# Kernel tuning notes

Hardware: AMD Instinct MI355X
Metric: run time of the kernel (lower is better)

## Reference

```python
import jax, jax.numpy as jnp
import numpy as np

B, H, S, D = 4, 16, 2048, 64


def setup_inputs() -> dict:
    key = jax.random.key(0)
    kq, kk, kv = jax.random.split(key, 3)
    Q = jax.random.normal(kq, (B, H, S, D), dtype=jnp.float32)
    K = jax.random.normal(kk, (B, H, S, D), dtype=jnp.float32)
    V = jax.random.normal(kv, (B, H, S, D), dtype=jnp.float32)
    mask = jnp.ones((1, 1, S, S), dtype=jnp.int32)
    return {"Q": Q, "K": K, "V": V, "mask": mask}


def reference(Q, K, V, mask):
    d_k = Q.shape[-1]
    scale = 1.0 / jnp.sqrt(jnp.asarray(d_k, dtype=Q.dtype))
    # [B, H, S, S] attention scores
    attn = jnp.einsum('bhqd,bhkd->bhqk', Q, K) * scale
    # mask == 0 -> -1e9 (matches torch boolean-index assignment)
    attn = jnp.where(mask == 0, jnp.asarray(-1e9, dtype=attn.dtype), attn)
    softmax_attn = jax.nn.softmax(attn, axis=-1)
    out = jnp.einsum('bhqk,bhkd->bhqd', softmax_attn, V)
    return out
```

## Files before the change

### kernel.cpp

```cpp
#include <hip/hip_runtime.h>

typedef __bf16 bf16;
typedef __attribute__((ext_vector_type(8))) __bf16 bf16x8;
typedef __attribute__((ext_vector_type(8))) ushort ushort8v;
typedef __attribute__((ext_vector_type(4))) ushort ushort4v;
typedef __attribute__((ext_vector_type(2))) uint uint2v;
typedef __attribute__((ext_vector_type(4))) float f32x4;

constexpr int S_LEN = 2048;
constexpr int DH    = 64;
constexpr int QBLK  = 128;
constexpr int KVBLK = 64;
constexpr int NWAVE = 4;
constexpr int NT    = S_LEN / KVBLK;
constexpr float QSCALE = 0.125f * 1.44269504088896f;
constexpr float NEG    = -1.44269504e9f;
constexpr float THR    = 8.0f;
constexpr size_t TILE_BYTES = (size_t)KVBLK * DH * 2;
constexpr size_t KV_BYTES   = (size_t)64 * NT * TILE_BYTES;

__device__ __forceinline__ ushort bfb(float f) {
  bf16 b = (bf16)f;
  return __builtin_bit_cast(ushort, b);
}
__device__ __forceinline__ int SWZ(int row) {
  return ((row & 7) ^ ((row >> 3) & 7)) << 4;
}
__device__ __forceinline__ uint cvtpk(float lo, float hi) {
  uint r;
  asm("v_cvt_pk_bf16_f32 %0, %1, %2" : "=v"(r) : "v"(lo), "v"(hi));
  return r;
}
__device__ __forceinline__ void gload16(const char* g, void* l) {
  __builtin_amdgcn_global_load_lds(
      (__attribute__((address_space(1))) void*)(g),
      (__attribute__((address_space(3))) void*)(l), 16, 0, 0);
}

__global__ __launch_bounds__(256)
void mask_flags(const int* __restrict__ M, uint* __restrict__ F) {
  const int qt = blockIdx.x;
  const int tid = threadIdx.x;
  const int r  = tid >> 2;
  const int c0 = (tid & 3) * 16;
  __shared__ int s[4];
  uint bits = 0;
  for (int kt = 0; kt < NT; ++kt) {
    const int* row = M + (size_t)(qt * 64 + r) * S_LEN + kt * 64 + c0;
    int ok = 1;
#pragma unroll
    for (int i = 0; i < 4; ++i) {
      int4 v = *(const int4*)(row + i * 4);
      ok &= (v.x != 0) & (v.y != 0) & (v.z != 0) & (v.w != 0);
    }
    ok = __all(ok) ? 1 : 0;
    if ((tid & 63) == 0) s[tid >> 6] = ok;
    __syncthreads();
    if (s[0] & s[1] & s[2] & s[3]) bits |= 1u << kt;
    __syncthreads();
  }
  if (tid == 0) F[qt] = bits;
}

__global__ __launch_bounds__(256)
void cvt_kv(const float* __restrict__ K, const float* __restrict__ V,
            char* __restrict__ kws, char* __restrict__ vws) {
  const int t = blockIdx.x, bh = blockIdx.y, tid = threadIdx.x;
  const float* Kb = K + ((size_t)bh * S_LEN + t * KVBLK) * DH;
  const float* Vb = V + ((size_t)bh * S_LEN + t * KVBLK) * DH;
  char* kd = kws + ((size_t)bh * NT + t) * TILE_BYTES;
  char* vd = vws + ((size_t)bh * NT + t) * TILE_BYTES;

  const int kr0 = tid >> 3, kc8 = tid & 7;
#pragma unroll
  for (int h = 0; h < 2; ++h) {
    const int row = kr0 + 32 * h;
    const float* kp = Kb + (size_t)row * DH + kc8 * 8;
    float4 a = *(const float4*)kp;
    float4 b = *(const float4*)(kp + 4);
    ushort8v pk;
    pk[0]=bfb(a.x); pk[1]=bfb(a.y); pk[2]=bfb(a.z); pk[3]=bfb(a.w);
    pk[4]=bfb(b.x); pk[5]=bfb(b.y); pk[6]=bfb(b.z); pk[7]=bfb(b.w);
    *(ushort8v*)(kd + row * 128 + ((kc8 * 16) ^ SWZ(row))) = pk;
  }
  const int vr = (tid >> 4) * 4, vc = (tid & 15) * 4;
  float rr[4][4];
#pragma unroll
  for (int i = 0; i < 4; ++i)
    *(float4*)rr[i] = *(const float4*)(Vb + (size_t)(vr + i) * DH + vc);
#pragma unroll
  for (int c = 0; c < 4; ++c) {
    const int d = vc + c;
    ushort4v p4;
    p4[0]=bfb(rr[0][c]); p4[1]=bfb(rr[1][c]);
    p4[2]=bfb(rr[2][c]); p4[3]=bfb(rr[3][c]);
    *(ushort4v*)(vd + d * 128 + ((vr * 2) ^ SWZ(d))) = p4;
  }
}

template<bool PRE>
__global__ __launch_bounds__(256, 4)
void attn_fwd(const float* __restrict__ Q, const float* __restrict__ K,
              const float* __restrict__ V, const int* __restrict__ M,
              const uint* __restrict__ F, const char* __restrict__ kws,
              const char* __restrict__ vws, float* __restrict__ O)
{
  __shared__ __align__(16) ushort kb[KVBLK * DH];
  __shared__ __align__(16) ushort vb[DH * KVBLK];
  __shared__ __align__(16) uint   pbw[NWAVE * 32 * 32];

  const int tid  = threadIdx.x;
  const int lane = tid & 63;
  const int w    = tid >> 6;
  const int qr   = lane & 15;
  const int kg   = lane >> 4;

  const int flat = blockIdx.y * gridDim.x + blockIdx.x;
  const int nid  = (flat & 7) * 128 + (flat >> 3);
  const int q0   = (nid & 15) * QBLK;
  const int bh   = nid >> 4;

  const float* Qb = Q + ((size_t)bh * S_LEN) * DH;
  const float* Kb = K + ((size_t)bh * S_LEN) * DH;
  const float* Vb = V + ((size_t)bh * S_LEN) * DH;

  const uint fmask = PRE ? (F[(q0 >> 6)] & F[(q0 >> 6) + 1]) : 0u;

  bf16x8 qf[2][2];
#pragma unroll
  for (int f = 0; f < 2; ++f) {
    const float* qp = Qb + (size_t)(q0 + w * 32 + f * 16 + qr) * DH + kg * 8;
#pragma unroll
    for (int ks = 0; ks < 2; ++ks) {
      float4 a = *(const float4*)(qp + ks * 32);
      float4 b = *(const float4*)(qp + ks * 32 + 4);
      bf16x8 t2;
      t2[0]=(bf16)(a.x*QSCALE); t2[1]=(bf16)(a.y*QSCALE);
      t2[2]=(bf16)(a.z*QSCALE); t2[3]=(bf16)(a.w*QSCALE);
      t2[4]=(bf16)(b.x*QSCALE); t2[5]=(bf16)(b.y*QSCALE);
      t2[6]=(bf16)(b.z*QSCALE); t2[7]=(bf16)(b.w*QSCALE);
      qf[f][ks] = t2;
    }
  }

  f32x4 acc[2][4];
#pragma unroll
  for (int f = 0; f < 2; ++f)
#pragma unroll
    for (int nt = 0; nt < 4; ++nt) { f32x4 z = {0.f,0.f,0.f,0.f}; acc[f][nt] = z; }
  float mrow[2] = {-1e30f, -1e30f};
  float rsum[2] = {0.f, 0.f};

  int lofs[4][2];
#pragma unroll
  for (int x = 0; x < 4; ++x) {
    const int row = 16 * x + qr;
    const int sw  = SWZ(row);
#pragma unroll
    for (int ks = 0; ks < 2; ++ks)
      lofs[x][ks] = row * 128 + ((kg * 16 + 64 * ks) ^ sw);
  }
  char* pb0 = (char*)pbw + (w * 32 + qr) * 128;
  char* pb1 = pb0 + 16 * 128;
  const int psw = (qr & 7) << 4;

  const int kr0 = tid >> 3, kc8 = tid & 7;
  const int vr = (tid >> 4) * 4, vc = (tid & 15) * 4;

  for (int t = 0; t < NT; ++t) {
    if (PRE) {
      const char* ksrc = kws + ((size_t)bh * NT + t) * TILE_BYTES;
      const char* vsrc = vws + ((size_t)bh * NT + t) * TILE_BYTES;
#pragma unroll
      for (int c = 0; c < 2; ++c) {
        const int off = (w + c * 4) * 1024 + lane * 16;
        gload16(ksrc + off, (char*)kb + off);
        gload16(vsrc + off, (char*)vb + off);
      }
    } else {
      const int kv0 = t * KVBLK;
#pragma unroll
      for (int h = 0; h < 2; ++h) {
        const int row = kr0 + 32 * h;
        const float* kp = Kb + (size_t)(kv0 + row) * DH + kc8 * 8;
        float4 a = *(const float4*)kp;
        float4 b = *(const float4*)(kp + 4);
        ushort8v pk;
        pk[0]=bfb(a.x); pk[1]=bfb(a.y); pk[2]=bfb(a.z); pk[3]=bfb(a.w);
        pk[4]=bfb(b.x); pk[5]=bfb(b.y); pk[6]=bfb(b.z); pk[7]=bfb(b.w);
        *(ushort8v*)((char*)kb + row * 128 + ((kc8 * 16) ^ SWZ(row))) = pk;
      }
      float rr[4][4];
#pragma unroll
      for (int i = 0; i < 4; ++i)
        *(float4*)rr[i] = *(const float4*)(Vb + (size_t)(kv0 + vr + i) * DH + vc);
#pragma unroll
      for (int c = 0; c < 4; ++c) {
        const int d = vc + c;
        ushort4v p4;
        p4[0]=bfb(rr[0][c]); p4[1]=bfb(rr[1][c]);
        p4[2]=bfb(rr[2][c]); p4[3]=bfb(rr[3][c]);
        *(ushort4v*)((char*)vb + d * 128 + ((vr * 2) ^ SWZ(d))) = p4;
      }
    }
    __syncthreads();

    f32x4 sc[2][4];
    __builtin_amdgcn_s_setprio(1);
#pragma unroll
    for (int ct = 0; ct < 4; ++ct) {
      f32x4 z = {0.f,0.f,0.f,0.f};
      sc[0][ct] = z; sc[1][ct] = z;
#pragma unroll
      for (int ks = 0; ks < 2; ++ks) {
        bf16x8 kf = *(const bf16x8*)((const char*)kb + lofs[ct][ks]);
        sc[0][ct] = __builtin_amdgcn_mfma_f32_16x16x32_bf16(kf, qf[0][ks], sc[0][ct], 0,0,0);
        sc[1][ct] = __builtin_amdgcn_mfma_f32_16x16x32_bf16(kf, qf[1][ks], sc[1][ct], 0,0,0);
      }
    }
    __builtin_amdgcn_s_setprio(0);

    const bool allset = PRE ? (((fmask >> t) & 1u) != 0u) : false;

#pragma unroll
    for (int f = 0; f < 2; ++f) {
      if (!allset) {
        const size_t mo = (size_t)(q0 + w * 32 + f * 16 + qr) * S_LEN
                          + t * KVBLK + 4 * kg;
#pragma unroll
        for (int ct = 0; ct < 4; ++ct)
#pragma unroll
          for (int r = 0; r < 4; ++r)
            if (M[mo + 16 * ct + r] == 0) sc[f][ct][r] = NEG;
      }

      float a0 = fmaxf(fmaxf(sc[f][0][0], sc[f][0][1]), sc[f][0][2]);
      float a1 = fmaxf(fmaxf(sc[f][0][3], sc[f][1][0]), sc[f][1][1]);
      float a2 = fmaxf(fmaxf(sc[f][1][2], sc[f][1][3]), sc[f][2][0]);
      float a3 = fmaxf(fmaxf(sc[f][2][1], sc[f][2][2]), sc[f][2][3]);
      float a4 = fmaxf(fmaxf(sc[f][3][0], sc[f][3][1]), sc[f][3][2]);
      float lm = fmaxf(fmaxf(a0, a1), a2);
      lm = fmaxf(fmaxf(lm, a3), a4);
      lm = fmaxf(lm, sc[f][3][3]);
      lm = fmaxf(lm, __shfl_xor(lm, 16));
      lm = fmaxf(lm, __shfl_xor(lm, 32));

      if (!__all(lm - mrow[f] <= THR)) {
        const float mnew = fmaxf(mrow[f], lm);
        const float corr = __builtin_amdgcn_exp2f(mrow[f] - mnew);
        rsum[f] *= corr;
#pragma unroll
        for (int nt = 0; nt < 4; ++nt) acc[f][nt] *= corr;
        mrow[f] = mnew;
      }

      float p[4][4];
      float ps = 0.f;
#pragma unroll
      for (int ct = 0; ct < 4; ++ct)
#pragma unroll
        for (int r = 0; r < 4; ++r) {
          p[ct][r] = __builtin_amdgcn_exp2f(sc[f][ct][r] - mrow[f]);
          ps += p[ct][r];
        }
      rsum[f] += ps;

      char* pb = f ? pb1 : pb0;
#pragma unroll
      for (int ct = 0; ct < 4; ++ct) {
        uint2v d2;
        d2[0] = cvtpk(p[ct][0], p[ct][1]);
        d2[1] = cvtpk(p[ct][2], p[ct][3]);
        *(uint2v*)(pb + ((32 * ct + 8 * kg) ^ psw)) = d2;
      }
    }

    __builtin_amdgcn_s_setprio(1);
#pragma unroll
    for (int ks = 0; ks < 2; ++ks) {
      bf16x8 pf0 = *(const bf16x8*)(pb0 + ((kg * 16 + 64 * ks) ^ psw));
      bf16x8 pf1 = *(const bf16x8*)(pb1 + ((kg * 16 + 64 * ks) ^ psw));
#pragma unroll
      for (int nt = 0; nt < 4; ++nt) {
        bf16x8 vf = *(const bf16x8*)((const char*)vb + lofs[nt][ks]);
        acc[0][nt] = __builtin_amdgcn_mfma_f32_16x16x32_bf16(vf, pf0, acc[0][nt], 0,0,0);
        acc[1][nt] = __builtin_amdgcn_mfma_f32_16x16x32_bf16(vf, pf1, acc[1][nt], 0,0,0);
      }
    }
    __builtin_amdgcn_s_setprio(0);

    __syncthreads();
  }

#pragma unroll
  for (int f = 0; f < 2; ++f) {
    float rs = rsum[f];
    rs += __shfl_xor(rs, 16);
    rs += __shfl_xor(rs, 32);
    const float inv = 1.0f / rs;
    float* Ob = O + ((size_t)bh * S_LEN + q0 + w * 32 + f * 16 + qr) * DH;
#pragma unroll
    for (int nt = 0; nt < 4; ++nt) {
      float4 o = { acc[f][nt][0] * inv, acc[f][nt][1] * inv,
                   acc[f][nt][2] * inv, acc[f][nt][3] * inv };
      *(float4*)(Ob + 16 * nt + 4 * kg) = o;
    }
  }
}

extern "C" void kernel_launch(void* const* d_in, const int* in_sizes, int n_in,
                              void* d_out, int out_size, void* d_ws, size_t ws_size,
                              hipStream_t stream)
{
  const float* Q = (const float*)d_in[0];
  const float* K = (const float*)d_in[1];
  const float* V = (const float*)d_in[2];
  const int*   M = (const int*)d_in[3];
  float* O = (float*)d_out;

  const size_t need = 4096 + 2 * KV_BYTES;
  const bool pre = (d_ws != nullptr) && (ws_size >= need);

  dim3 grid(S_LEN / QBLK, 4 * 16);
  if (pre) {
    uint* F   = (uint*)d_ws;
    char* kws = (char*)d_ws + 4096;
    char* vws = kws + KV_BYTES;
    mask_flags<<<32, 256, 0, stream>>>(M, F);
    cvt_kv<<<dim3(NT, 64), 256, 0, stream>>>(K, V, kws, vws);
    attn_fwd<true><<<grid, NWAVE * 64, 0, stream>>>(Q, K, V, M, F, kws, vws, O);
  } else {
    attn_fwd<false><<<grid, NWAVE * 64, 0, stream>>>(Q, K, V, M, nullptr, nullptr, nullptr, O);
  }
}
```

Measured before the change: 138.8 us.

## Double-buffer K/V LDS tiles with async loads and parallelize mask flag scan

The attention kernel now keeps two LDS buffers for K and V. It issues the async global-to-LDS load for the next tile before computing on the current one, so load latency overlaps MFMA work. The mask_flags prepass is split across 8 key-tile groups per query tile, with the partial bitmasks combined by atomicOr after a memset, which gives it more parallelism. Doubling the K/V LDS footprint lowers the occupancy hint from 4 to 3 blocks per CU, and the change adds a memset launch.

After: 137.8 us. No clear change (-0.7%).

```diff
diff --git a/kernel.cpp b/kernel.cpp
--- a/kernel.cpp
+++ b/kernel.cpp
@@ -39,18 +39,20 @@
 
 __global__ __launch_bounds__(256)
 void mask_flags(const int* __restrict__ M, uint* __restrict__ F) {
-  const int qt = blockIdx.x;
+  const int qt  = blockIdx.x;
+  const int kt0 = blockIdx.y * 4;
   const int tid = threadIdx.x;
   const int r  = tid >> 2;
   const int c0 = (tid & 3) * 16;
   __shared__ int s[4];
   uint bits = 0;
-  for (int kt = 0; kt < NT; ++kt) {
+  for (int i = 0; i < 4; ++i) {
+    const int kt = kt0 + i;
     const int* row = M + (size_t)(qt * 64 + r) * S_LEN + kt * 64 + c0;
     int ok = 1;
 #pragma unroll
-    for (int i = 0; i < 4; ++i) {
-      int4 v = *(const int4*)(row + i * 4);
+    for (int j = 0; j < 4; ++j) {
+      int4 v = *(const int4*)(row + j * 4);
       ok &= (v.x != 0) & (v.y != 0) & (v.z != 0) & (v.w != 0);
     }
     ok = __all(ok) ? 1 : 0;
@@ -59,7 +61,7 @@
     if (s[0] & s[1] & s[2] & s[3]) bits |= 1u << kt;
     __syncthreads();
   }
-  if (tid == 0) F[qt] = bits;
+  if (tid == 0) atomicOr(&F[qt], bits);
 }
 
 __global__ __launch_bounds__(256)
@@ -99,14 +101,14 @@
 }
 
 template<bool PRE>
-__global__ __launch_bounds__(256, 4)
+__global__ __launch_bounds__(256, 3)
 void attn_fwd(const float* __restrict__ Q, const float* __restrict__ K,
               const float* __restrict__ V, const int* __restrict__ M,
               const uint* __restrict__ F, const char* __restrict__ kws,
               const char* __restrict__ vws, float* __restrict__ O)
 {
-  __shared__ __align__(16) ushort kb[KVBLK * DH];
-  __shared__ __align__(16) ushort vb[DH * KVBLK];
+  __shared__ __align__(16) ushort kb[2][KVBLK * DH];
+  __shared__ __align__(16) ushort vb[2][DH * KVBLK];
   __shared__ __align__(16) uint   pbw[NWAVE * 32 * 32];
 
   const int tid  = threadIdx.x;
@@ -167,44 +169,7 @@
   const int kr0 = tid >> 3, kc8 = tid & 7;
   const int vr = (tid >> 4) * 4, vc = (tid & 15) * 4;
 
-  for (int t = 0; t < NT; ++t) {
-    if (PRE) {
-      const char* ksrc = kws + ((size_t)bh * NT + t) * TILE_BYTES;
-      const char* vsrc = vws + ((size_t)bh * NT + t) * TILE_BYTES;
-#pragma unroll
-      for (int c = 0; c < 2; ++c) {
-        const int off = (w + c * 4) * 1024 + lane * 16;
-        gload16(ksrc + off, (char*)kb + off);
-        gload16(vsrc + off, (char*)vb + off);
-      }
-    } else {
-      const int kv0 = t * KVBLK;
-#pragma unroll
-      for (int h = 0; h < 2; ++h) {
-        const int row = kr0 + 32 * h;
-        const float* kp = Kb + (size_t)(kv0 + row) * DH + kc8 * 8;
-        float4 a = *(const float4*)kp;
-        float4 b = *(const float4*)(kp + 4);
-        ushort8v pk;
-        pk[0]=bfb(a.x); pk[1]=bfb(a.y); pk[2]=bfb(a.z); pk[3]=bfb(a.w);
-        pk[4]=bfb(b.x); pk[5]=bfb(b.y); pk[6]=bfb(b.z); pk[7]=bfb(b.w);
-        *(ushort8v*)((char*)kb + row * 128 + ((kc8 * 16) ^ SWZ(row))) = pk;
-      }
-      float rr[4][4];
-#pragma unroll
-      for (int i = 0; i < 4; ++i)
-        *(float4*)rr[i] = *(const float4*)(Vb + (size_t)(kv0 + vr + i) * DH + vc);
-#pragma unroll
-      for (int c = 0; c < 4; ++c) {
-        const int d = vc + c;
-        ushort4v p4;
-        p4[0]=bfb(rr[0][c]); p4[1]=bfb(rr[1][c]);
-        p4[2]=bfb(rr[2][c]); p4[3]=bfb(rr[3][c]);
-        *(ushort4v*)((char*)vb + d * 128 + ((vr * 2) ^ SWZ(d))) = p4;
-      }
-    }
-    __syncthreads();
-
+  auto compute = [&](int t, const char* kbB, const char* vbB) {
     f32x4 sc[2][4];
     __builtin_amdgcn_s_setprio(1);
 #pragma unroll
@@ -213,7 +178,7 @@
       sc[0][ct] = z; sc[1][ct] = z;
 #pragma unroll
       for (int ks = 0; ks < 2; ++ks) {
-        bf16x8 kf = *(const bf16x8*)((const char*)kb + lofs[ct][ks]);
+        bf16x8 kf = *(const bf16x8*)(kbB + lofs[ct][ks]);
         sc[0][ct] = __builtin_amdgcn_mfma_f32_16x16x32_bf16(kf, qf[0][ks], sc[0][ct], 0,0,0);
         sc[1][ct] = __builtin_amdgcn_mfma_f32_16x16x32_bf16(kf, qf[1][ks], sc[1][ct], 0,0,0);
       }
@@ -282,14 +247,66 @@
       bf16x8 pf1 = *(const bf16x8*)(pb1 + ((kg * 16 + 64 * ks) ^ psw));
 #pragma unroll
       for (int nt = 0; nt < 4; ++nt) {
-        bf16x8 vf = *(const bf16x8*)((const char*)vb + lofs[nt][ks]);
+        bf16x8 vf = *(const bf16x8*)(vbB + lofs[nt][ks]);
         acc[0][nt] = __builtin_amdgcn_mfma_f32_16x16x32_bf16(vf, pf0, acc[0][nt], 0,0,0);
         acc[1][nt] = __builtin_amdgcn_mfma_f32_16x16x32_bf16(vf, pf1, acc[1][nt], 0,0,0);
       }
     }
     __builtin_amdgcn_s_setprio(0);
-
+  };
+
+  if constexpr (PRE) {
+    auto issue = [&](int b, int t) {
+      const char* ksrc = kws + ((size_t)bh * NT + t) * TILE_BYTES;
+      const char* vsrc = vws + ((size_t)bh * NT + t) * TILE_BYTES;
+#pragma unroll
+      for (int c = 0; c < 2; ++c) {
+        const int off = (w + c * 4) * 1024 + lane * 16;
+        gload16(ksrc + off, (char*)kb[b] + off);
+        gload16(vsrc + off, (char*)vb[b] + off);
+      }
+    };
+
+    issue(0, 0);
     __syncthreads();
+    for (int t = 0; t < NT; t += 2) {
+      issue(1, t + 1);
+      compute(t, (const char*)kb[0], (const char*)vb[0]);
+      __syncthreads();
+      if (t + 2 < NT) issue(0, t + 2);
+      compute(t + 1, (const char*)kb[1], (const char*)vb[1]);
+      __syncthreads();
+    }
+  } else {
+    for (int t = 0; t < NT; ++t) {
+      const int kv0 = t * KVBLK;
+#pragma unroll
+      for (int h = 0; h < 2; ++h) {
+        const int row = kr0 + 32 * h;
+        const float* kp = Kb + (size_t)(kv0 + row) * DH + kc8 * 8;
+        float4 a = *(const float4*)kp;
+        float4 b = *(const float4*)(kp + 4);
+        ushort8v pk;
+        pk[0]=bfb(a.x); pk[1]=bfb(a.y); pk[2]=bfb(a.z); pk[3]=bfb(a.w);
+        pk[4]=bfb(b.x); pk[5]=bfb(b.y); pk[6]=bfb(b.z); pk[7]=bfb(b.w);
+        *(ushort8v*)((char*)kb[0] + row * 128 + ((kc8 * 16) ^ SWZ(row))) = pk;
+      }
+      float rr[4][4];
+#pragma unroll
+      for (int i = 0; i < 4; ++i)
+        *(float4*)rr[i] = *(const float4*)(Vb + (size_t)(kv0 + vr + i) * DH + vc);
+#pragma unroll
+      for (int c = 0; c < 4; ++c) {
+        const int d = vc + c;
+        ushort4v p4;
+        p4[0]=bfb(rr[0][c]); p4[1]=bfb(rr[1][c]);
+        p4[2]=bfb(rr[2][c]); p4[3]=bfb(rr[3][c]);
+        *(ushort4v*)((char*)vb[0] + d * 128 + ((vr * 2) ^ SWZ(d))) = p4;
+      }
+      __syncthreads();
+      compute(t, (const char*)kb[0], (const char*)vb[0]);
+      __syncthreads();
+    }
   }
 
 #pragma unroll
@@ -326,7 +343,8 @@
     uint* F   = (uint*)d_ws;
     char* kws = (char*)d_ws + 4096;
     char* vws = kws + KV_BYTES;
-    mask_flags<<<32, 256, 0, stream>>>(M, F);
+    hipMemsetAsync(F, 0, 32 * sizeof(uint), stream);
+    mask_flags<<<dim3(32, 8), 256, 0, stream>>>(M, F);
     cvt_kv<<<dim3(NT, 64), 256, 0, stream>>>(K, V, kws, vws);
     attn_fwd<true><<<grid, NWAVE * 64, 0, stream>>>(Q, K, V, M, F, kws, vws, O);
   } else {
```

## Restructure attention into single-wave blocks reading pre-converted K/V directly from global

Applied to the files above, without the earlier changes.

The main attention kernel becomes a 64-thread, single-wave block that handles 64 query rows. It reads the pre-swizzled bf16 K/V tiles straight from global memory into registers, which removes the LDS staging and the per-tile block barriers. The mask-flag kernel is parallelised over key tiles with atomicOr after a memset, and the non-workspace path keeps the old kernel as a fallback. The trade is more register pressure from four row fragments and no K/V sharing in LDS across waves, which leans on the caches instead.

Result: faster. 126.4 us (-8.9%).

```diff
diff --git a/kernel.cpp b/kernel.cpp
--- a/kernel.cpp
+++ b/kernel.cpp
@@ -9,10 +9,9 @@
 
 constexpr int S_LEN = 2048;
 constexpr int DH    = 64;
-constexpr int QBLK  = 128;
 constexpr int KVBLK = 64;
-constexpr int NWAVE = 4;
 constexpr int NT    = S_LEN / KVBLK;
+constexpr int QW    = 64;
 constexpr float QSCALE = 0.125f * 1.44269504088896f;
 constexpr float NEG    = -1.44269504e9f;
 constexpr float THR    = 8.0f;
@@ -31,26 +30,23 @@
   asm("v_cvt_pk_bf16_f32 %0, %1, %2" : "=v"(r) : "v"(lo), "v"(hi));
   return r;
 }
-__device__ __forceinline__ void gload16(const char* g, void* l) {
-  __builtin_amdgcn_global_load_lds(
-      (__attribute__((address_space(1))) void*)(g),
-      (__attribute__((address_space(3))) void*)(l), 16, 0, 0);
-}
 
 __global__ __launch_bounds__(256)
 void mask_flags(const int* __restrict__ M, uint* __restrict__ F) {
-  const int qt = blockIdx.x;
+  const int qt  = blockIdx.x;
+  const int kt0 = blockIdx.y * 4;
   const int tid = threadIdx.x;
   const int r  = tid >> 2;
   const int c0 = (tid & 3) * 16;
   __shared__ int s[4];
   uint bits = 0;
-  for (int kt = 0; kt < NT; ++kt) {
+  for (int i = 0; i < 4; ++i) {
+    const int kt = kt0 + i;
     const int* row = M + (size_t)(qt * 64 + r) * S_LEN + kt * 64 + c0;
     int ok = 1;
 #pragma unroll
-    for (int i = 0; i < 4; ++i) {
-      int4 v = *(const int4*)(row + i * 4);
+    for (int j = 0; j < 4; ++j) {
+      int4 v = *(const int4*)(row + j * 4);
       ok &= (v.x != 0) & (v.y != 0) & (v.z != 0) & (v.w != 0);
     }
     ok = __all(ok) ? 1 : 0;
@@ -59,7 +55,7 @@
     if (s[0] & s[1] & s[2] & s[3]) bits |= 1u << kt;
     __syncthreads();
   }
-  if (tid == 0) F[qt] = bits;
+  if (tid == 0) atomicOr(&F[qt], bits);
 }
 
 __global__ __launch_bounds__(256)
@@ -98,38 +94,32 @@
   }
 }
 
-template<bool PRE>
-__global__ __launch_bounds__(256, 4)
-void attn_fwd(const float* __restrict__ Q, const float* __restrict__ K,
-              const float* __restrict__ V, const int* __restrict__ M,
-              const uint* __restrict__ F, const char* __restrict__ kws,
-              const char* __restrict__ vws, float* __restrict__ O)
+__global__ __launch_bounds__(64, 2)
+void attn_fwd_direct(const float* __restrict__ Q, const int* __restrict__ M,
+                     const uint* __restrict__ F, const char* __restrict__ kws,
+                     const char* __restrict__ vws, float* __restrict__ O)
 {
-  __shared__ __align__(16) ushort kb[KVBLK * DH];
-  __shared__ __align__(16) ushort vb[DH * KVBLK];
-  __shared__ __align__(16) uint   pbw[NWAVE * 32 * 32];
-
-  const int tid  = threadIdx.x;
-  const int lane = tid & 63;
-  const int w    = tid >> 6;
+  __shared__ __align__(16) uint pbw[QW * 32];
+
+  const int lane = threadIdx.x & 63;
   const int qr   = lane & 15;
   const int kg   = lane >> 4;
 
-  const int flat = blockIdx.y * gridDim.x + blockIdx.x;
-  const int nid  = (flat & 7) * 128 + (flat >> 3);
-  const int q0   = (nid & 15) * QBLK;
-  const int bh   = nid >> 4;
-
-  const float* Qb = Q + ((size_t)bh * S_LEN) * DH;
-  const float* Kb = K + ((size_t)bh * S_LEN) * DH;
-  const float* Vb = V + ((size_t)bh * S_LEN) * DH;
-
-  const uint fmask = PRE ? (F[(q0 >> 6)] & F[(q0 >> 6) + 1]) : 0u;
-
-  bf16x8 qf[2][2];
-#pragma unroll
-  for (int f = 0; f < 2; ++f) {
-    const float* qp = Qb + (size_t)(q0 + w * 32 + f * 16 + qr) * DH + kg * 8;
+  const int bid = blockIdx.x;
+  const int nid = (bid & 7) * 256 + (bid >> 3);
+  const int q0  = (nid & 31) * QW;
+  const int bh  = nid >> 5;
+
+  const float* Qb = Q + (size_t)bh * S_LEN * DH;
+  const uint fmask = F[q0 >> 6];
+
+  const char* kbase = kws + (size_t)bh * NT * TILE_BYTES;
+  const char* vbase = vws + (size_t)bh * NT * TILE_BYTES;
+
+  bf16x8 qf[4][2];
+#pragma unroll
+  for (int f = 0; f < 4; ++f) {
+    const float* qp = Qb + (size_t)(q0 + f * 16 + qr) * DH + kg * 8;
 #pragma unroll
     for (int ks = 0; ks < 2; ++ks) {
       float4 a = *(const float4*)(qp + ks * 32);
@@ -143,13 +133,13 @@
     }
   }
 
-  f32x4 acc[2][4];
-#pragma unroll
-  for (int f = 0; f < 2; ++f)
+  f32x4 acc[4][4];
+#pragma unroll
+  for (int f = 0; f < 4; ++f)
 #pragma unroll
     for (int nt = 0; nt < 4; ++nt) { f32x4 z = {0.f,0.f,0.f,0.f}; acc[f][nt] = z; }
-  float mrow[2] = {-1e30f, -1e30f};
-  float rsum[2] = {0.f, 0.f};
+  float mrow[4] = {-1e30f,-1e30f,-1e30f,-1e30f};
+  float rsum[4] = {0.f,0.f,0.f,0.f};
 
   int lofs[4][2];
 #pragma unroll
@@ -160,73 +150,44 @@
     for (int ks = 0; ks < 2; ++ks)
       lofs[x][ks] = row * 128 + ((kg * 16 + 64 * ks) ^ sw);
   }
-  char* pb0 = (char*)pbw + (w * 32 + qr) * 128;
-  char* pb1 = pb0 + 16 * 128;
   const int psw = (qr & 7) << 4;
 
-  const int kr0 = tid >> 3, kc8 = tid & 7;
-  const int vr = (tid >> 4) * 4, vc = (tid & 15) * 4;
-
   for (int t = 0; t < NT; ++t) {
-    if (PRE) {
-      const char* ksrc = kws + ((size_t)bh * NT + t) * TILE_BYTES;
-      const char* vsrc = vws + ((size_t)bh * NT + t) * TILE_BYTES;
-#pragma unroll
-      for (int c = 0; c < 2; ++c) {
-        const int off = (w + c * 4) * 1024 + lane * 16;
-        gload16(ksrc + off, (char*)kb + off);
-        gload16(vsrc + off, (char*)vb + off);
-      }
-    } else {
-      const int kv0 = t * KVBLK;
-#pragma unroll
-      for (int h = 0; h < 2; ++h) {
-        const int row = kr0 + 32 * h;
-        const float* kp = Kb + (size_t)(kv0 + row) * DH + kc8 * 8;
-        float4 a = *(const float4*)kp;
-        float4 b = *(const float4*)(kp + 4);
-        ushort8v pk;
-        pk[0]=bfb(a.x); pk[1]=bfb(a.y); pk[2]=bfb(a.z); pk[3]=bfb(a.w);
-        pk[4]=bfb(b.x); pk[5]=bfb(b.y); pk[6]=bfb(b.z); pk[7]=bfb(b.w);
-        *(ushort8v*)((char*)kb + row * 128 + ((kc8 * 16) ^ SWZ(row))) = pk;
-      }
-      float rr[4][4];
-#pragma unroll
-      for (int i = 0; i < 4; ++i)
-        *(float4*)rr[i] = *(const float4*)(Vb + (size_t)(kv0 + vr + i) * DH + vc);
-#pragma unroll
-      for (int c = 0; c < 4; ++c) {
-        const int d = vc + c;
-        ushort4v p4;
-        p4[0]=bfb(rr[0][c]); p4[1]=bfb(rr[1][c]);
-        p4[2]=bfb(rr[2][c]); p4[3]=bfb(rr[3][c]);
-        *(ushort4v*)((char*)vb + d * 128 + ((vr * 2) ^ SWZ(d))) = p4;
-      }
-    }
-    __syncthreads();
-
-    f32x4 sc[2][4];
+    const char* kt = kbase + (size_t)t * TILE_BYTES;
+    const char* vt = vbase + (size_t)t * TILE_BYTES;
+
+    f32x4 sc[4][4];
+#pragma unroll
+    for (int f = 0; f < 4; ++f)
+#pragma unroll
+      for (int ct = 0; ct < 4; ++ct) { f32x4 z = {0.f,0.f,0.f,0.f}; sc[f][ct] = z; }
+
     __builtin_amdgcn_s_setprio(1);
 #pragma unroll
-    for (int ct = 0; ct < 4; ++ct) {
-      f32x4 z = {0.f,0.f,0.f,0.f};
-      sc[0][ct] = z; sc[1][ct] = z;
+    for (int ct = 0; ct < 4; ++ct)
 #pragma unroll
       for (int ks = 0; ks < 2; ++ks) {
-        bf16x8 kf = *(const bf16x8*)((const char*)kb + lofs[ct][ks]);
+        bf16x8 kf = *(const bf16x8*)(kt + lofs[ct][ks]);
         sc[0][ct] = __builtin_amdgcn_mfma_f32_16x16x32_bf16(kf, qf[0][ks], sc[0][ct], 0,0,0);
         sc[1][ct] = __builtin_amdgcn_mfma_f32_16x16x32_bf16(kf, qf[1][ks], sc[1][ct], 0,0,0);
-      }
-    }
+        sc[2][ct] = __builtin_amdgcn_mfma_f32_16x16x32_bf16(kf, qf[2][ks], sc[2][ct], 0,0,0);
+        sc[3][ct] = __builtin_amdgcn_mfma_f32_16x16x32_bf16(kf, qf[3][ks], sc[3][ct], 0,0,0);
+      }
     __builtin_amdgcn_s_setprio(0);
 
-    const bool allset = PRE ? (((fmask >> t) & 1u) != 0u) : false;
-
-#pragma unroll
-    for (int f = 0; f < 2; ++f) {
+    bf16x8 vfr[4][2];
+#pragma unroll
+    for (int nt = 0; nt < 4; ++nt)
+#pragma unroll
+      for (int ks = 0; ks < 2; ++ks)
+        vfr[nt][ks] = *(const bf16x8*)(vt + lofs[nt][ks]);
+
+    const bool allset = ((fmask >> t) & 1u) != 0u;
+
+#pragma unroll
+    for (int f = 0; f < 4; ++f) {
       if (!allset) {
-        const size_t mo = (size_t)(q0 + w * 32 + f * 16 + qr) * S_LEN
-                          + t * KVBLK + 4 * kg;
+        const size_t mo = (size_t)(q0 + f * 16 + qr) * S_LEN + t * KVBLK + 4 * kg;
 #pragma unroll
         for (int ct = 0; ct < 4; ++ct)
 #pragma unroll
@@ -265,7 +226,7 @@
         }
       rsum[f] += ps;
 
-      char* pb = f ? pb1 : pb0;
+      char* pb = (char*)pbw + (f * 16 + qr) * 128;
 #pragma unroll
       for (int ct = 0; ct < 4; ++ct) {
         uint2v d2;
@@ -278,6 +239,195 @@
     __builtin_amdgcn_s_setprio(1);
 #pragma unroll
     for (int ks = 0; ks < 2; ++ks) {
+      bf16x8 pf0 = *(const bf16x8*)((char*)pbw + (0 * 16 + qr) * 128 + ((kg * 16 + 64 * ks) ^ psw));
+      bf16x8 pf1 = *(const bf16x8*)((char*)pbw + (1 * 16 + qr) * 128 + ((kg * 16 + 64 * ks) ^ psw));
+      bf16x8 pf2 = *(const bf16x8*)((char*)pbw + (2 * 16 + qr) * 128 + ((kg * 16 + 64 * ks) ^ psw));
+      bf16x8 pf3 = *(const bf16x8*)((char*)pbw + (3 * 16 + qr) * 128 + ((kg * 16 + 64 * ks) ^ psw));
+#pragma unroll
+      for (int nt = 0; nt < 4; ++nt) {
+        bf16x8 vf = vfr[nt][ks];
+        acc[0][nt] = __builtin_amdgcn_mfma_f32_16x16x32_bf16(vf, pf0, acc[0][nt], 0,0,0);
+        acc[1][nt] = __builtin_amdgcn_mfma_f32_16x16x32_bf16(vf, pf1, acc[1][nt], 0,0,0);
+        acc[2][nt] = __builtin_amdgcn_mfma_f32_16x16x32_bf16(vf, pf2, acc[2][nt], 0,0,0);
+        acc[3][nt] = __builtin_amdgcn_mfma_f32_16x16x32_bf16(vf, pf3, acc[3][nt], 0,0,0);
+      }
+    }
+    __builtin_amdgcn_s_setprio(0);
+  }
+
+#pragma unroll
+  for (int f = 0; f < 4; ++f) {
+    float rs = rsum[f];
+    rs += __shfl_xor(rs, 16);
+    rs += __shfl_xor(rs, 32);
+    const float inv = 1.0f / rs;
+    float* Ob = O + ((size_t)bh * S_LEN + q0 + f * 16 + qr) * DH;
+#pragma unroll
+    for (int nt = 0; nt < 4; ++nt) {
+      float4 o = { acc[f][nt][0] * inv, acc[f][nt][1] * inv,
+                   acc[f][nt][2] * inv, acc[f][nt][3] * inv };
+      *(float4*)(Ob + 16 * nt + 4 * kg) = o;
+    }
+  }
+}
+
+__global__ __launch_bounds__(256, 4)
+void attn_fwd_fb(const float* __restrict__ Q, const float* __restrict__ K,
+                 const float* __restrict__ V, const int* __restrict__ M,
+                 float* __restrict__ O)
+{
+  __shared__ __align__(16) ushort kb[KVBLK * DH];
+  __shared__ __align__(16) ushort vb[DH * KVBLK];
+  __shared__ __align__(16) uint   pbw[4 * 32 * 32];
+
+  const int tid  = threadIdx.x;
+  const int lane = tid & 63;
+  const int w    = tid >> 6;
+  const int qr   = lane & 15;
+  const int kg   = lane >> 4;
+
+  const int flat = blockIdx.y * gridDim.x + blockIdx.x;
+  const int nid  = (flat & 7) * 128 + (flat >> 3);
+  const int q0   = (nid & 15) * 128;
+  const int bh   = nid >> 4;
+
+  const float* Qb = Q + ((size_t)bh * S_LEN) * DH;
+  const float* Kb = K + ((size_t)bh * S_LEN) * DH;
+  const float* Vb = V + ((size_t)bh * S_LEN) * DH;
+
+  bf16x8 qf[2][2];
+#pragma unroll
+  for (int f = 0; f < 2; ++f) {
+    const float* qp = Qb + (size_t)(q0 + w * 32 + f * 16 + qr) * DH + kg * 8;
+#pragma unroll
+    for (int ks = 0; ks < 2; ++ks) {
+      float4 a = *(const float4*)(qp + ks * 32);
+      float4 b = *(const float4*)(qp + ks * 32 + 4);
+      bf16x8 t2;
+      t2[0]=(bf16)(a.x*QSCALE); t2[1]=(bf16)(a.y*QSCALE);
+      t2[2]=(bf16)(a.z*QSCALE); t2[3]=(bf16)(a.w*QSCALE);
+      t2[4]=(bf16)(b.x*QSCALE); t2[5]=(bf16)(b.y*QSCALE);
+      t2[6]=(bf16)(b.z*QSCALE); t2[7]=(bf16)(b.w*QSCALE);
+      qf[f][ks] = t2;
+    }
+  }
+
+  f32x4 acc[2][4];
+#pragma unroll
+  for (int f = 0; f < 2; ++f)
+#pragma unroll
+    for (int nt = 0; nt < 4; ++nt) { f32x4 z = {0.f,0.f,0.f,0.f}; acc[f][nt] = z; }
+  float mrow[2] = {-1e30f, -1e30f};
+  float rsum[2] = {0.f, 0.f};
+
+  int lofs[4][2];
+#pragma unroll
+  for (int x = 0; x < 4; ++x) {
+    const int row = 16 * x + qr;
+    const int sw  = SWZ(row);
+#pragma unroll
+    for (int ks = 0; ks < 2; ++ks)
+      lofs[x][ks] = row * 128 + ((kg * 16 + 64 * ks) ^ sw);
+  }
+  char* pb0 = (char*)pbw + (w * 32 + qr) * 128;
+  char* pb1 = pb0 + 16 * 128;
+  const int psw = (qr & 7) << 4;
+
+  const int kr0 = tid >> 3, kc8 = tid & 7;
+  const int vr = (tid >> 4) * 4, vc = (tid & 15) * 4;
+
+  for (int t = 0; t < NT; ++t) {
+    const int kv0 = t * KVBLK;
+#pragma unroll
+    for (int h = 0; h < 2; ++h) {
+      const int row = kr0 + 32 * h;
+      const float* kp = Kb + (size_t)(kv0 + row) * DH + kc8 * 8;
+      float4 a = *(const float4*)kp;
+      float4 b = *(const float4*)(kp + 4);
+      ushort8v pk;
+      pk[0]=bfb(a.x); pk[1]=bfb(a.y); pk[2]=bfb(a.z); pk[3]=bfb(a.w);
+      pk[4]=bfb(b.x); pk[5]=bfb(b.y); pk[6]=bfb(b.z); pk[7]=bfb(b.w);
+      *(ushort8v*)((char*)kb + row * 128 + ((kc8 * 16) ^ SWZ(row))) = pk;
+    }
+    float rr[4][4];
+#pragma unroll
+    for (int i = 0; i < 4; ++i)
+      *(float4*)rr[i] = *(const float4*)(Vb + (size_t)(kv0 + vr + i) * DH + vc);
+#pragma unroll
+    for (int c = 0; c < 4; ++c) {
+      const int d = vc + c;
+      ushort4v p4;
+      p4[0]=bfb(rr[0][c]); p4[1]=bfb(rr[1][c]);
+      p4[2]=bfb(rr[2][c]); p4[3]=bfb(rr[3][c]);
+      *(ushort4v*)((char*)vb + d * 128 + ((vr * 2) ^ SWZ(d))) = p4;
+    }
+    __syncthreads();
+
+    f32x4 sc[2][4];
+#pragma unroll
+    for (int ct = 0; ct < 4; ++ct) {
+      f32x4 z = {0.f,0.f,0.f,0.f};
+      sc[0][ct] = z; sc[1][ct] = z;
+#pragma unroll
+      for (int ks = 0; ks < 2; ++ks) {
+        bf16x8 kf = *(const bf16x8*)((const char*)kb + lofs[ct][ks]);
+        sc[0][ct] = __builtin_amdgcn_mfma_f32_16x16x32_bf16(kf, qf[0][ks], sc[0][ct], 0,0,0);
+        sc[1][ct] = __builtin_amdgcn_mfma_f32_16x16x32_bf16(kf, qf[1][ks], sc[1][ct], 0,0,0);
+      }
+    }
+
+#pragma unroll
+    for (int f = 0; f < 2; ++f) {
+      const size_t mo = (size_t)(q0 + w * 32 + f * 16 + qr) * S_LEN + t * KVBLK + 4 * kg;
+#pragma unroll
+      for (int ct = 0; ct < 4; ++ct)
+#pragma unroll
+        for (int r = 0; r < 4; ++r)
+          if (M[mo + 16 * ct + r] == 0) sc[f][ct][r] = NEG;
+
+      float a0 = fmaxf(fmaxf(sc[f][0][0], sc[f][0][1]), sc[f][0][2]);
+      float a1 = fmaxf(fmaxf(sc[f][0][3], sc[f][1][0]), sc[f][1][1]);
+      float a2 = fmaxf(fmaxf(sc[f][1][2], sc[f][1][3]), sc[f][2][0]);
+      float a3 = fmaxf(fmaxf(sc[f][2][1], sc[f][2][2]), sc[f][2][3]);
+      float a4 = fmaxf(fmaxf(sc[f][3][0], sc[f][3][1]), sc[f][3][2]);
+      float lm = fmaxf(fmaxf(a0, a1), a2);
+      lm = fmaxf(fmaxf(lm, a3), a4);
+      lm = fmaxf(lm, sc[f][3][3]);
+      lm = fmaxf(lm, __shfl_xor(lm, 16));
+      lm = fmaxf(lm, __shfl_xor(lm, 32));
+
+      if (!__all(lm - mrow[f] <= THR)) {
+        const float mnew = fmaxf(mrow[f], lm);
+        const float corr = __builtin_amdgcn_exp2f(mrow[f] - mnew);
+        rsum[f] *= corr;
+#pragma unroll
+        for (int nt = 0; nt < 4; ++nt) acc[f][nt] *= corr;
+        mrow[f] = mnew;
+      }
+
+      float p[4][4];
+      float ps = 0.f;
+#pragma unroll
+      for (int ct = 0; ct < 4; ++ct)
+#pragma unroll
+        for (int r = 0; r < 4; ++r) {
+          p[ct][r] = __builtin_amdgcn_exp2f(sc[f][ct][r] - mrow[f]);
+          ps += p[ct][r];
+        }
+      rsum[f] += ps;
+
+      char* pb = f ? pb1 : pb0;
+#pragma unroll
+      for (int ct = 0; ct < 4; ++ct) {
+        uint2v d2;
+        d2[0] = cvtpk(p[ct][0], p[ct][1]);
+        d2[1] = cvtpk(p[ct][2], p[ct][3]);
+        *(uint2v*)(pb + ((32 * ct + 8 * kg) ^ psw)) = d2;
+      }
+    }
+
+#pragma unroll
+    for (int ks = 0; ks < 2; ++ks) {
       bf16x8 pf0 = *(const bf16x8*)(pb0 + ((kg * 16 + 64 * ks) ^ psw));
       bf16x8 pf1 = *(const bf16x8*)(pb1 + ((kg * 16 + 64 * ks) ^ psw));
 #pragma unroll
@@ -287,8 +437,6 @@
         acc[1][nt] = __builtin_amdgcn_mfma_f32_16x16x32_bf16(vf, pf1, acc[1][nt], 0,0,0);
       }
     }
-    __builtin_amdgcn_s_setprio(0);
-
     __syncthreads();
   }
 
@@ -321,15 +469,15 @@
   const size_t need = 4096 + 2 * KV_BYTES;
   const bool pre = (d_ws != nullptr) && (ws_size >= need);
 
-  dim3 grid(S_LEN / QBLK, 4 * 16);
   if (pre) {
     uint* F   = (uint*)d_ws;
     char* kws = (char*)d_ws + 4096;
     char* vws = kws + KV_BYTES;
-    mask_flags<<<32, 256, 0, stream>>>(M, F);
+    hipMemsetAsync(F, 0, 32 * sizeof(uint), stream);
+    mask_flags<<<dim3(32, 8), 256, 0, stream>>>(M, F);
     cvt_kv<<<dim3(NT, 64), 256, 0, stream>>>(K, V, kws, vws);
-    attn_fwd<true><<<grid, NWAVE * 64, 0, stream>>>(Q, K, V, M, F, kws, vws, O);
+    attn_fwd_direct<<<2048, 64, 0, stream>>>(Q, M, F, kws, vws, O);
   } else {
-    attn_fwd<false><<<grid, NWAVE * 64, 0, stream>>>(Q, K, V, M, nullptr, nullptr, nullptr, O);
-  }
-}
+    attn_fwd_fb<<<dim3(16, 64), 256, 0, stream>>>(Q, K, V, M, O);
+  }
+}
```
